# Performance work log

Hardware: AMD Instinct MI355X
Metric: run time of the kernel (lower is better)

The kernel has to match this reference:

```python
import jax, jax.numpy as jnp
import numpy as np

NUM_HEADS = 16


def _qdq(x):
    """Symmetric int8 fake-quant along the last axis (per-token for
    activations, per-output-channel for [out,in] weights). Equivalent math to
    int8 GEMM with dynamic scales: (x_q @ w_q.T) * sx * sw == qdq(x) @ qdq(w).T."""
    s = jnp.maximum(jnp.max(jnp.abs(x), axis=-1, keepdims=True) / 127.0, 1e-8)
    return jnp.clip(jnp.round(x / s), -127.0, 127.0) * s


def setup_inputs() -> dict:
    key = jax.random.key(0)
    ks = jax.random.split(key, 8)
    B, N, M, D = 2, 4096, 512, 2048
    w_std = 0.02
    return {
        "x": jax.random.normal(ks[0], (B, N, D), jnp.float32),
        "cond": jax.random.normal(ks[1], (B, M, D), jnp.float32),
        "wq": jax.random.normal(ks[2], (D, D), jnp.float32) * w_std,
        "bq": jax.random.normal(ks[3], (D,), jnp.float32) * w_std,
        "wkv": jax.random.normal(ks[4], (2 * D, D), jnp.float32) * w_std,
        "bkv": jax.random.normal(ks[5], (2 * D,), jnp.float32) * w_std,
        "wp": jax.random.normal(ks[6], (D, D), jnp.float32) * w_std,
        "bp": jax.random.normal(ks[7], (D,), jnp.float32) * w_std,
    }


def reference(x, cond, wq, bq, wkv, bkv, wp, bp):
    B, N, C = x.shape
    M = cond.shape[1]
    H = NUM_HEADS
    Dh = C // H

    # W8A8 dynamic-scale q projection (per-token act quant, per-channel weight quant)
    q = _qdq(x) @ _qdq(wq).T + bq                      # [B,N,C]
    # fp16-style kv projection
    kv = cond @ wkv.T + bkv                            # [B,M,2C]
    k, v = jnp.split(kv, 2, axis=-1)                   # view(...,2,H,Dh).unbind(2)

    q = q.reshape(B, N, H, Dh)
    k = k.reshape(B, M, H, Dh)
    v = v.reshape(B, M, H, Dh)

    scale = 1.0 / np.sqrt(Dh)
    attn = jax.nn.softmax(jnp.einsum('bnhd,bmhd->bhnm', q, k) * scale, axis=-1)
    o = jnp.einsum('bhnm,bmhd->bnhd', attn, v).reshape(B, N, C)

    # fused quant_sum (per-token requant of attention output) + W8A8 proj
    out = _qdq(o) @ _qdq(wp).T + bp                    # [B,N,C]
    return out
```

## Files before the change

### kernel.cpp

```cpp
#include <hip/hip_runtime.h>
#include <cstdint>
#include <cstddef>


typedef __bf16 bf16_t;
typedef __bf16 bf16x8 __attribute__((ext_vector_type(8)));
typedef float f32x4 __attribute__((ext_vector_type(4)));

__device__ __forceinline__ void gld16(void* lds, const void* g) {
    __builtin_amdgcn_global_load_lds(
        (__attribute__((address_space(1))) uint32_t*)(uintptr_t)g,
        (__attribute__((address_space(3))) uint32_t*)(uint32_t)(uintptr_t)lds,
        16, 0, 0);
}

__device__ __forceinline__ void load8(const float* p, int i, float* v) {
    const float4* p4 = (const float4*)p;
    float4 a = p4[2 * i], b = p4[2 * i + 1];
    v[0] = a.x; v[1] = a.y; v[2] = a.z; v[3] = a.w;
    v[4] = b.x; v[5] = b.y; v[6] = b.z; v[7] = b.w;
}
__device__ __forceinline__ void load8(const bf16_t* p, int i, float* v) {
    bf16x8 t = ((const bf16x8*)p)[i];
#pragma unroll
    for (int j = 0; j < 8; ++j) v[j] = (float)t[j];
}

template <int QUANT, typename T>
__global__ __launch_bounds__(256) void rowpack(const T* __restrict__ in,
                                               bf16_t* __restrict__ out, int K) {
    const int tid = threadIdx.x;
    const size_t row = blockIdx.x;
    const T* rp = in + row * (size_t)K;
    const int n8 = K >> 3;
    float scale = 1.0f;
    if (QUANT) {
        float m = 0.f;
        for (int i = tid; i < n8; i += 256) {
            float v[8];
            load8(rp, i, v);
#pragma unroll
            for (int j = 0; j < 8; ++j) m = fmaxf(m, fabsf(v[j]));
        }
        __shared__ float red[256];
        red[tid] = m;
        __syncthreads();
        for (int s = 128; s > 0; s >>= 1) {
            if (tid < s) red[tid] = fmaxf(red[tid], red[tid + s]);
            __syncthreads();
        }
        scale = fmaxf(red[0] * (1.0f / 127.0f), 1e-8f);
    }
    const int KT = K >> 5;
    const int p = (int)(row >> 7), c = ((int)row >> 4) & 7, lm = (int)row & 15;
    for (int i = tid; i < n8; i += 256) {
        const int col = i << 3;
        const int kt = col >> 5, quad = (col >> 3) & 3;
        float v[8];
        load8(rp, i, v);
        bf16x8 o8;
#pragma unroll
        for (int j = 0; j < 8; ++j) {
            float q = v[j];
            if (QUANT) {
                q = rintf(q / scale);
                q = fminf(127.f, fmaxf(-127.f, q)) * scale;
            }
            o8[j] = (bf16_t)q;
        }
        const size_t dst = ((size_t)(p * KT + kt) * 8 + c) * 512 + (quad * 16 + lm) * 8;
        *(bf16x8*)(out + dst) = o8;
    }
}

template <int MODE>
__device__ __forceinline__ void epi_store(void* C, int N, int row, int col, float v) {
    if (MODE == 1) {
        ((float*)C)[(size_t)row * N + col] = v;
    } else if (MODE == 0) {
        const int b = row >> 12, n = row & 4095;
        const int h = col >> 7, d = col & 127;
        const int p = n >> 6, mt = (n >> 4) & 3, lmq = n & 15;
        const int kq = d >> 5, qq = (d >> 3) & 3, jq = d & 7;
        const size_t idx = (((size_t)(b * 16 + h) * 64 + p) * 16 + kq * 4 + mt) * 512 +
                           (qq * 16 + lmq) * 8 + jq;
        ((bf16_t*)C)[idx] = (bf16_t)v;
    } else {
        const int b = row >> 9, m = row & 511;
        const int half = col >> 11, h = (col >> 7) & 15, d = col & 127;
        const int t8 = m >> 6;
        bf16_t* out = (bf16_t*)C;
        if (half == 0) {
            const int nt = (m >> 4) & 3, lmk = m & 15;
            const int kc = d >> 5, qk = (d >> 3) & 3, jk = d & 7;
            const size_t idx = (((size_t)(b * 16 + h) * 8 + t8) * 16 + kc * 4 + nt) * 512 +
                               (qk * 16 + lmk) * 8 + jk;
            out[idx] = (bf16_t)v;
        } else {
            const int kv2 = (m >> 5) & 1, qv = (m >> 3) & 3, jv = m & 7;
            const int ntv = d >> 4, lmv = d & 15;
            const size_t idx = 2097152 +
                (((size_t)(b * 16 + h) * 8 + t8) * 16 + kv2 * 8 + ntv) * 512 +
                (qv * 16 + lmv) * 8 + jv;
            out[idx] = (bf16_t)v;
        }
    }
}

__device__ __forceinline__ void stage_tile256(const bf16_t* __restrict__ A,
                                              const bf16_t* __restrict__ B,
                                              bf16_t* sa, bf16_t* sb,
                                              int pa, int pb, int KT, int t,
                                              int w, int l) {
#pragma unroll
    for (int it = 0; it < 4; ++it) {
        const int ci = w * 4 + it;
        const int h = ci >> 4, kt2 = (ci >> 3) & 1, c = ci & 7;
        const size_t ga = (((size_t)(pa + h) * KT + (2 * t + kt2)) * 8 + c) * 512 + l * 8;
        const size_t gb = (((size_t)(pb + h) * KT + (2 * t + kt2)) * 8 + c) * 512 + l * 8;
        gld16(sa + ci * 512, A + ga);
        gld16(sb + ci * 512, B + gb);
    }
}

template <int MODE>
__global__ __launch_bounds__(512, 1) void gemm_pk8(const bf16_t* __restrict__ A,
                                                   const bf16_t* __restrict__ B,
                                                   const float* __restrict__ bias,
                                                   void* __restrict__ C,
                                                   int N, int K) {
    __shared__ __align__(16) bf16_t sA[2][16384];
    __shared__ __align__(16) bf16_t sB[2][16384];

    const int tid = threadIdx.x;
    const int l = tid & 63, w = tid >> 6;
    const int lm = l & 15, quad = l >> 4;
    const int wm = w & 1, wn = w >> 1;

    const int nwg = gridDim.x;
    const int bid = blockIdx.x;
    const int s = (bid & 7) * (nwg >> 3) + (bid >> 3);
    const int bx = s & 7, by = s >> 3;

    const int KT = K >> 5;
    const int NT = K >> 6;
    const int pa = by * 2, pb = bx * 2;

    stage_tile256(A, B, sA[0], sB[0], pa, pb, KT, 0, w, l);
    __builtin_amdgcn_sched_barrier(0);
    stage_tile256(A, B, sA[1], sB[1], pa, pb, KT, 1, w, l);
    asm volatile("s_waitcnt vmcnt(8)" ::: "memory");
    __builtin_amdgcn_s_barrier();

    f32x4 acc[8][4] = {};

    for (int t = 0; t < NT; ++t) {
        const bf16_t* sa = sA[t & 1];
        const bf16_t* sb = sB[t & 1];
        bf16x8 bfr[4][2];
        bf16x8 af[2][2];

#pragma unroll
        for (int j = 0; j < 4; ++j)
#pragma unroll
            for (int k2 = 0; k2 < 2; ++k2)
                bfr[j][k2] = *(const bf16x8*)(
                    sb + ((((wn >> 1) * 2 + k2) * 8 + (wn & 1) * 4 + j) * 512) + l * 8);
#pragma unroll
        for (int ii = 0; ii < 2; ++ii)
#pragma unroll
            for (int k2 = 0; k2 < 2; ++k2)
                af[ii][k2] = *(const bf16x8*)(sa + (((wm * 2 + k2) * 8 + ii) * 512) + l * 8);
        __builtin_amdgcn_s_barrier();
        asm volatile("s_waitcnt lgkmcnt(0)" ::: "memory");
        __builtin_amdgcn_sched_barrier(0);
        __builtin_amdgcn_s_setprio(1);
#pragma unroll
        for (int ii = 0; ii < 2; ++ii)
#pragma unroll
            for (int j = 0; j < 4; ++j)
#pragma unroll
                for (int k2 = 0; k2 < 2; ++k2)
                    acc[ii][j] = __builtin_amdgcn_mfma_f32_16x16x32_bf16(
                        af[ii][k2], bfr[j][k2], acc[ii][j], 0, 0, 0);
        __builtin_amdgcn_s_setprio(0);
        __builtin_amdgcn_s_barrier();

#pragma unroll
        for (int q = 1; q <= 2; ++q) {
#pragma unroll
            for (int ii = 0; ii < 2; ++ii)
#pragma unroll
                for (int k2 = 0; k2 < 2; ++k2)
                    af[ii][k2] = *(const bf16x8*)(
                        sa + (((wm * 2 + k2) * 8 + (q * 2 + ii)) * 512) + l * 8);
            __builtin_amdgcn_s_barrier();
            asm volatile("s_waitcnt lgkmcnt(0)" ::: "memory");
            __builtin_amdgcn_sched_barrier(0);
            __builtin_amdgcn_s_setprio(1);
#pragma unroll
            for (int ii = 0; ii < 2; ++ii)
#pragma unroll
                for (int j = 0; j < 4; ++j)
#pragma unroll
                    for (int k2 = 0; k2 < 2; ++k2)
                        acc[q * 2 + ii][j] = __builtin_amdgcn_mfma_f32_16x16x32_bf16(
                            af[ii][k2], bfr[j][k2], acc[q * 2 + ii][j], 0, 0, 0);
            __builtin_amdgcn_s_setprio(0);
            __builtin_amdgcn_s_barrier();
        }

#pragma unroll
        for (int ii = 0; ii < 2; ++ii)
#pragma unroll
            for (int k2 = 0; k2 < 2; ++k2)
                af[ii][k2] = *(const bf16x8*)(
                    sa + (((wm * 2 + k2) * 8 + (6 + ii)) * 512) + l * 8);
        asm volatile("s_waitcnt lgkmcnt(0)" ::: "memory");
        __builtin_amdgcn_s_barrier();
        if (t + 2 < NT)
            stage_tile256(A, B, sA[t & 1], sB[t & 1], pa, pb, KT, t + 2, w, l);
        __builtin_amdgcn_sched_barrier(0);
        __builtin_amdgcn_s_setprio(1);
#pragma unroll
        for (int ii = 0; ii < 2; ++ii)
#pragma unroll
            for (int j = 0; j < 4; ++j)
#pragma unroll
                for (int k2 = 0; k2 < 2; ++k2)
                    acc[6 + ii][j] = __builtin_amdgcn_mfma_f32_16x16x32_bf16(
                        af[ii][k2], bfr[j][k2], acc[6 + ii][j], 0, 0, 0);
        __builtin_amdgcn_s_setprio(0);
        if (t + 2 < NT)
            asm volatile("s_waitcnt vmcnt(8)" ::: "memory");
        else
            asm volatile("s_waitcnt vmcnt(0)" ::: "memory");
        __builtin_amdgcn_s_barrier();
    }

#pragma unroll
    for (int i = 0; i < 8; ++i) {
#pragma unroll
        for (int j = 0; j < 4; ++j) {
            const int col = bx * 256 + wn * 64 + j * 16 + lm;
            const float bv = bias[col];
#pragma unroll
            for (int r = 0; r < 4; ++r) {
                const int row = by * 256 + wm * 128 + i * 16 + quad * 4 + r;
                epi_store<MODE>(C, N, row, col, acc[i][j][r] + bv);
            }
        }
    }
}

__global__ __launch_bounds__(256) void gemm_kv(const bf16_t* __restrict__ A,
                                               const bf16_t* __restrict__ B,
                                               const float* __restrict__ bias,
                                               bf16_t* __restrict__ C,
                                               int N, int K) {
    __shared__ __align__(16) bf16_t sA[4096];
    __shared__ __align__(16) bf16_t sB[8192];

    const int tid = threadIdx.x;
    const int l = tid & 63, w = tid >> 6;
    const int lm = l & 15, quad = l >> 4;
    const int wm = w & 1, wn = w >> 1;
    const int KT = K >> 5;
    const int p = blockIdx.y >> 1, hh = blockIdx.y & 1;
    const size_t aPan = (size_t)p * KT * 8 * 512;
    const size_t bBase = (size_t)blockIdx.x * KT * 8 * 512;

    f32x4 acc[2][4] = {};
    const int NIT = K >> 6;
    for (int kt = 0; kt < NIT; ++kt) {
        __syncthreads();
#pragma unroll
        for (int it = 0; it < 2; ++it) {
            const int lc = it * 4 + w;
            const int s = lc >> 2, cc = lc & 3;
            gld16(sA + lc * 512,
                  A + aPan + ((size_t)(kt * 2 + s) * 8 + hh * 4 + cc) * 512 + l * 8);
        }
#pragma unroll
        for (int it = 0; it < 4; ++it) {
            const int lc = it * 4 + w;
            gld16(sB + lc * 512, B + bBase + ((size_t)kt * 16 + lc) * 512 + l * 8);
        }
        __syncthreads();
#pragma unroll
        for (int s = 0; s < 2; ++s) {
            bf16x8 af[2], bfr[4];
#pragma unroll
            for (int i = 0; i < 2; ++i)
                af[i] = *(const bf16x8*)(sA + (s * 4 + wm * 2 + i) * 512 + l * 8);
#pragma unroll
            for (int j = 0; j < 4; ++j)
                bfr[j] = *(const bf16x8*)(sB + (s * 8 + wn * 4 + j) * 512 + l * 8);
#pragma unroll
            for (int i = 0; i < 2; ++i)
#pragma unroll
                for (int j = 0; j < 4; ++j)
                    acc[i][j] =
                        __builtin_amdgcn_mfma_f32_16x16x32_bf16(af[i], bfr[j], acc[i][j], 0, 0, 0);
        }
    }
#pragma unroll
    for (int i = 0; i < 2; ++i) {
#pragma unroll
        for (int j = 0; j < 4; ++j) {
            const int col = blockIdx.x * 128 + wn * 64 + j * 16 + lm;
            const float bv = bias[col];
#pragma unroll
            for (int r = 0; r < 4; ++r) {
                const int row = blockIdx.y * 64 + wm * 32 + i * 16 + quad * 4 + r;
                epi_store<2>(C, N, row, col, acc[i][j][r] + bv);
            }
        }
    }
}

__global__ __launch_bounds__(256, 2) void attn64(const bf16_t* __restrict__ qpk,
                                                 const bf16_t* __restrict__ kvpk,
                                                 bf16_t* __restrict__ o) {
    constexpr float SCALE = 0.08838834764831845f;
    __shared__ __align__(16) bf16_t sQP[8192];
    __shared__ __align__(16) bf16_t sKV[16384];
    __shared__ float redM[4][64];
    __shared__ float redS[4][64];

    const int tid = threadIdx.x;
    const int l = tid & 63, w = tid >> 6;
    const int lm = l & 15, quad = l >> 4;
    const int b = blockIdx.z, h = blockIdx.y;
    const int p = blockIdx.x;
    const int bh = b * 16 + h;
    const size_t qbase = ((size_t)bh * 64 + p) * 8192;
    const size_t kbase = (size_t)bh * 65536;
    const size_t vbase = 2097152 + (size_t)bh * 65536;

#pragma unroll
    for (int it = 0; it < 4; ++it) {
        const int c = it * 4 + w;
        gld16(sQP + c * 512, qpk + qbase + (size_t)c * 512 + l * 8);
    }
#pragma unroll
    for (int it = 0; it < 4; ++it) {
        const int c = it * 4 + w;
        gld16(sKV + c * 512, kvpk + kbase + (size_t)c * 512 + l * 8);
    }

    f32x4 sfr[8][4] = {};
#pragma unroll
    for (int sg = 0; sg < 8; ++sg) {
        if (sg < 7) {
            bf16_t* kn = sKV + (((sg + 1) & 1) << 13);
#pragma unroll
            for (int it = 0; it < 4; ++it) {
                const int c = it * 4 + w;
                gld16(kn + c * 512, kvpk + kbase + ((size_t)(sg + 1) * 16 + c) * 512 + l * 8);
            }
            asm volatile("s_waitcnt vmcnt(4)" ::: "memory");
        } else {
            asm volatile("s_waitcnt vmcnt(0)" ::: "memory");
        }
        __builtin_amdgcn_s_barrier();
        const bf16_t* kb = sKV + ((sg & 1) << 13);
        __builtin_amdgcn_s_setprio(1);
#pragma unroll
        for (int kc = 0; kc < 4; ++kc) {
            bf16x8 bb = *(const bf16x8*)(kb + (kc * 4 + w) * 512 + l * 8);
#pragma unroll
            for (int mt = 0; mt < 4; ++mt) {
                bf16x8 aa = *(const bf16x8*)(sQP + (kc * 4 + mt) * 512 + l * 8);
                sfr[sg][mt] =
                    __builtin_amdgcn_mfma_f32_16x16x32_bf16(aa, bb, sfr[sg][mt], 0, 0, 0);
            }
        }
        __builtin_amdgcn_s_setprio(0);
        asm volatile("s_waitcnt lgkmcnt(0)" ::: "memory");
        __builtin_amdgcn_s_barrier();
    }

#pragma unroll
    for (int it = 0; it < 4; ++it) {
        const int c = it * 4 + w;
        gld16(sKV + c * 512, kvpk + vbase + (size_t)c * 512 + l * 8);
    }

    float inv[4][4];
    {
        float mymax[4][4];
#pragma unroll
        for (int mt = 0; mt < 4; ++mt)
#pragma unroll
            for (int r = 0; r < 4; ++r) {
                float m = -3.0e38f;
#pragma unroll
                for (int t8 = 0; t8 < 8; ++t8) m = fmaxf(m, sfr[t8][mt][r]);
                m = fmaxf(m, __shfl_xor(m, 1));
                m = fmaxf(m, __shfl_xor(m, 2));
                m = fmaxf(m, __shfl_xor(m, 4));
                m = fmaxf(m, __shfl_xor(m, 8));
                mymax[mt][r] = m;
            }
        if (lm == 0) {
#pragma unroll
            for (int mt = 0; mt < 4; ++mt)
#pragma unroll
                for (int r = 0; r < 4; ++r)
                    redM[w][mt * 16 + quad * 4 + r] = mymax[mt][r];
        }
        asm volatile("s_waitcnt lgkmcnt(0)" ::: "memory");
        __builtin_amdgcn_s_barrier();
#pragma unroll
        for (int mt = 0; mt < 4; ++mt)
#pragma unroll
            for (int r = 0; r < 4; ++r) {
                const int row = mt * 16 + quad * 4 + r;
                const float M =
                    fmaxf(fmaxf(redM[0][row], redM[1][row]), fmaxf(redM[2][row], redM[3][row])) *
                    SCALE;
                float s = 0.f;
#pragma unroll
                for (int t8 = 0; t8 < 8; ++t8) {
                    const float pe = __expf(sfr[t8][mt][r] * SCALE - M);
                    sfr[t8][mt][r] = pe;
                    s += pe;
                }
                s += __shfl_xor(s, 1);
                s += __shfl_xor(s, 2);
                s += __shfl_xor(s, 4);
                s += __shfl_xor(s, 8);
                if (lm == 0) redS[w][row] = s;
            }
        asm volatile("s_waitcnt lgkmcnt(0)" ::: "memory");
        __builtin_amdgcn_s_barrier();
#pragma unroll
        for (int mt = 0; mt < 4; ++mt)
#pragma unroll
            for (int r = 0; r < 4; ++r) {
                const int row = mt * 16 + quad * 4 + r;
                inv[mt][r] = 1.f / (redS[0][row] + redS[1][row] + redS[2][row] + redS[3][row]);
            }
    }

    const int kvh = w >> 1;
    const int quadp = (w & 1) * 2 + (lm >> 3);
    const int jd = lm & 7;
#define PWRITE(sg_) do {                                                          \
    const int r8_ = ((sg_) & 1) * 8;                                              \
    _Pragma("unroll") for (int mt = 0; mt < 4; ++mt)                              \
    _Pragma("unroll") for (int r = 0; r < 4; ++r)                                 \
        sQP[(r8_ + mt * 2 + kvh) * 512 + (quadp * 16 + quad * 4 + r) * 8 + jd] =  \
            (bf16_t)sfr[sg_][mt][r];                                              \
} while (0)

    f32x4 oc[4][2] = {};
    PWRITE(0);
#pragma unroll
    for (int sg = 0; sg < 8; ++sg) {
        if (sg < 7) {
            bf16_t* vn = sKV + (((sg + 1) & 1) << 13);
#pragma unroll
            for (int it = 0; it < 4; ++it) {
                const int c = it * 4 + w;
                gld16(vn + c * 512, kvpk + vbase + ((size_t)(sg + 1) * 16 + c) * 512 + l * 8);
            }
            PWRITE(sg + 1);
            asm volatile("s_waitcnt vmcnt(4)" ::: "memory");
        } else {
            asm volatile("s_waitcnt vmcnt(0)" ::: "memory");
        }
        asm volatile("s_waitcnt lgkmcnt(0)" ::: "memory");
        __builtin_amdgcn_s_barrier();
        const bf16_t* vb = sKV + ((sg & 1) << 13);
        const bf16_t* pb = sQP + ((sg & 1) << 12);
        __builtin_amdgcn_s_setprio(1);
#pragma unroll
        for (int kvf2 = 0; kvf2 < 2; ++kvf2) {
            bf16x8 aa[4];
#pragma unroll
            for (int mt = 0; mt < 4; ++mt)
                aa[mt] = *(const bf16x8*)(pb + (mt * 2 + kvf2) * 512 + l * 8);
#pragma unroll
            for (int ni = 0; ni < 2; ++ni) {
                bf16x8 bb = *(const bf16x8*)(vb + (kvf2 * 8 + w * 2 + ni) * 512 + l * 8);
#pragma unroll
                for (int mt = 0; mt < 4; ++mt)
                    oc[mt][ni] =
                        __builtin_amdgcn_mfma_f32_16x16x32_bf16(aa[mt], bb, oc[mt][ni], 0, 0, 0);
            }
        }
        __builtin_amdgcn_s_setprio(0);
        asm volatile("s_waitcnt lgkmcnt(0)" ::: "memory");
        __builtin_amdgcn_s_barrier();
    }
#undef PWRITE

#pragma unroll
    for (int mt = 0; mt < 4; ++mt)
#pragma unroll
        for (int ni = 0; ni < 2; ++ni)
#pragma unroll
            for (int r = 0; r < 4; ++r) {
                const int row = mt * 16 + quad * 4 + r;
                const int d = w * 32 + ni * 16 + lm;
                o[((size_t)b * 4096 + p * 64 + row) * 2048 + h * 128 + d] =
                    (bf16_t)(oc[mt][ni][r] * inv[mt][r]);
            }
}

extern "C" void kernel_launch(void* const* d_in, const int* in_sizes, int n_in,
                              void* d_out, int out_size, void* d_ws, size_t ws_size,
                              hipStream_t stream) {
    (void)in_sizes; (void)n_in; (void)out_size; (void)ws_size;
    const float* x    = (const float*)d_in[0];
    const float* cond = (const float*)d_in[1];
    const float* wq   = (const float*)d_in[2];
    const float* bq   = (const float*)d_in[3];
    const float* wkv  = (const float*)d_in[4];
    const float* bkv  = (const float*)d_in[5];
    const float* wp   = (const float*)d_in[6];
    const float* bp   = (const float*)d_in[7];

    const size_t MB = 1ull << 20;
    uint8_t* ws = (uint8_t*)d_ws;
    bf16_t* qxpk   = (bf16_t*)(ws + 0);
    bf16_t* qpk    = (bf16_t*)(ws + 32 * MB);
    bf16_t* wqpk   = (bf16_t*)(ws + 64 * MB);
    bf16_t* wkvpk  = (bf16_t*)(ws + 72 * MB);
    bf16_t* wppk   = (bf16_t*)(ws + 88 * MB);
    bf16_t* condpk = (bf16_t*)(ws + 96 * MB);
    bf16_t* kvpk   = (bf16_t*)(ws + 100 * MB);
    bf16_t* o_nat  = qxpk;
    bf16_t* opk    = qpk;

    dim3 blk(256);
    rowpack<1, float><<<8192, blk, 0, stream>>>(x, qxpk, 2048);
    rowpack<1, float><<<2048, blk, 0, stream>>>(wq, wqpk, 2048);
    rowpack<1, float><<<2048, blk, 0, stream>>>(wp, wppk, 2048);
    rowpack<0, float><<<1024, blk, 0, stream>>>(cond, condpk, 2048);
    rowpack<0, float><<<4096, blk, 0, stream>>>(wkv, wkvpk, 2048);
    gemm_pk8<0><<<dim3(256), dim3(512), 0, stream>>>(qxpk, wqpk, bq, qpk, 2048, 2048);
    gemm_kv<<<dim3(32, 16), blk, 0, stream>>>(condpk, wkvpk, bkv, kvpk, 4096, 2048);
    attn64<<<dim3(64, 16, 2), blk, 0, stream>>>(qpk, kvpk, o_nat);
    rowpack<1, bf16_t><<<8192, blk, 0, stream>>>(o_nat, opk, 2048);
    gemm_pk8<1><<<dim3(256), dim3(512), 0, stream>>>(opk, wppk, bp, (float*)d_out, 2048, 2048);
}
```

Before: 513.0 us.

## Triple-buffer K/V stream in attention kernel and hoist Q fragments to registers

Replaces the two-stage K/V shared-memory double buffer with a three-stage ring that keeps two tiles in flight, and runs K and V as one continuous prefetch stream so V loads start during the QK phase. Q fragments are loaded once into registers instead of being re-read from shared memory on every K tile. The cost is more shared memory (48KB for sKV) and extra VGPRs for the Q fragments, which may lower occupancy under the 2-block launch bound.

```diff
diff --git a/kernel.cpp b/kernel.cpp
--- a/kernel.cpp
+++ b/kernel.cpp
@@ -324,7 +324,7 @@
                                                  bf16_t* __restrict__ o) {
     constexpr float SCALE = 0.08838834764831845f;
     __shared__ __align__(16) bf16_t sQP[8192];
-    __shared__ __align__(16) bf16_t sKV[16384];
+    __shared__ __align__(16) bf16_t sKV[24576];
     __shared__ float redM[4][64];
     __shared__ float redS[4][64];
 
@@ -338,53 +338,55 @@
     const size_t kbase = (size_t)bh * 65536;
     const size_t vbase = 2097152 + (size_t)bh * 65536;
 
+    auto issue = [&](int n) {
+        bf16_t* dst = sKV + (n % 3) * 8192;
+        const size_t src = (n < 8) ? kbase + (size_t)n * 8192
+                                   : vbase + (size_t)(n - 8) * 8192;
+#pragma unroll
+        for (int it = 0; it < 4; ++it) {
+            const int c = it * 4 + w;
+            gld16(dst + c * 512, kvpk + src + (size_t)c * 512 + l * 8);
+        }
+    };
+
 #pragma unroll
     for (int it = 0; it < 4; ++it) {
         const int c = it * 4 + w;
         gld16(sQP + c * 512, qpk + qbase + (size_t)c * 512 + l * 8);
     }
-#pragma unroll
-    for (int it = 0; it < 4; ++it) {
-        const int c = it * 4 + w;
-        gld16(sKV + c * 512, kvpk + kbase + (size_t)c * 512 + l * 8);
-    }
-
+    issue(0);
+    __builtin_amdgcn_sched_barrier(0);
+    issue(1);
+
+    bf16x8 qf[4][4];
     f32x4 sfr[8][4] = {};
+
 #pragma unroll
     for (int sg = 0; sg < 8; ++sg) {
-        if (sg < 7) {
-            bf16_t* kn = sKV + (((sg + 1) & 1) << 13);
-#pragma unroll
-            for (int it = 0; it < 4; ++it) {
-                const int c = it * 4 + w;
-                gld16(kn + c * 512, kvpk + kbase + ((size_t)(sg + 1) * 16 + c) * 512 + l * 8);
-            }
-            asm volatile("s_waitcnt vmcnt(4)" ::: "memory");
-        } else {
-            asm volatile("s_waitcnt vmcnt(0)" ::: "memory");
-        }
-        __builtin_amdgcn_s_barrier();
-        const bf16_t* kb = sKV + ((sg & 1) << 13);
+        issue(sg + 2);
+        asm volatile("s_waitcnt vmcnt(8)" ::: "memory");
+        __builtin_amdgcn_s_barrier();
+        __builtin_amdgcn_sched_barrier(0);
+        const bf16_t* kb = sKV + (sg % 3) * 8192;
+        if (sg == 0) {
+#pragma unroll
+            for (int kc = 0; kc < 4; ++kc)
+#pragma unroll
+                for (int mt = 0; mt < 4; ++mt)
+                    qf[kc][mt] = *(const bf16x8*)(sQP + (kc * 4 + mt) * 512 + l * 8);
+        }
         __builtin_amdgcn_s_setprio(1);
 #pragma unroll
         for (int kc = 0; kc < 4; ++kc) {
             bf16x8 bb = *(const bf16x8*)(kb + (kc * 4 + w) * 512 + l * 8);
 #pragma unroll
-            for (int mt = 0; mt < 4; ++mt) {
-                bf16x8 aa = *(const bf16x8*)(sQP + (kc * 4 + mt) * 512 + l * 8);
+            for (int mt = 0; mt < 4; ++mt)
                 sfr[sg][mt] =
-                    __builtin_amdgcn_mfma_f32_16x16x32_bf16(aa, bb, sfr[sg][mt], 0, 0, 0);
-            }
+                    __builtin_amdgcn_mfma_f32_16x16x32_bf16(qf[kc][mt], bb, sfr[sg][mt], 0, 0, 0);
         }
         __builtin_amdgcn_s_setprio(0);
         asm volatile("s_waitcnt lgkmcnt(0)" ::: "memory");
         __builtin_amdgcn_s_barrier();
-    }
-
-#pragma unroll
-    for (int it = 0; it < 4; ++it) {
-        const int c = it * 4 + w;
-        gld16(sKV + c * 512, kvpk + vbase + (size_t)c * 512 + l * 8);
     }
 
     float inv[4][4];
@@ -459,21 +461,18 @@
     PWRITE(0);
 #pragma unroll
     for (int sg = 0; sg < 8; ++sg) {
-        if (sg < 7) {
-            bf16_t* vn = sKV + (((sg + 1) & 1) << 13);
-#pragma unroll
-            for (int it = 0; it < 4; ++it) {
-                const int c = it * 4 + w;
-                gld16(vn + c * 512, kvpk + vbase + ((size_t)(sg + 1) * 16 + c) * 512 + l * 8);
-            }
-            PWRITE(sg + 1);
+        if (sg < 6) issue(sg + 10);
+        if (sg < 7) PWRITE(sg + 1);
+        if (sg < 6)
+            asm volatile("s_waitcnt vmcnt(8)" ::: "memory");
+        else if (sg == 6)
             asm volatile("s_waitcnt vmcnt(4)" ::: "memory");
-        } else {
+        else
             asm volatile("s_waitcnt vmcnt(0)" ::: "memory");
-        }
-        asm volatile("s_waitcnt lgkmcnt(0)" ::: "memory");
-        __builtin_amdgcn_s_barrier();
-        const bf16_t* vb = sKV + ((sg & 1) << 13);
+        asm volatile("s_waitcnt lgkmcnt(0)" ::: "memory");
+        __builtin_amdgcn_s_barrier();
+        __builtin_amdgcn_sched_barrier(0);
+        const bf16_t* vb = sKV + ((sg + 8) % 3) * 8192;
         const bf16_t* pb = sQP + ((sg & 1) << 12);
         __builtin_amdgcn_s_setprio(1);
 #pragma unroll
```

Result: no change. 512.6 us (-0.1%).

## Deepen K/V prefetch in attention, drop per-step barriers, raise occupancy

Applied to the files above, without the earlier changes.

The attention kernel now prefetches K and V tiles two stages ahead. It relies on each wave loading the same LDS chunks it later reads, so most block-wide barriers in the QK and PV loops can be removed. Operand fragments are read into registers before the next tile is issued. Softmax probabilities are packed into bf16 pairs in 32-bit registers instead of staying in the fp32 score array, and launch bounds ask for 3 blocks per CU instead of 2. The goal is to hide global-load latency and cut synchronisation stalls, at the cost of higher register pressure and a possible spill under the tighter occupancy target.

```diff
diff --git a/kernel.cpp b/kernel.cpp
--- a/kernel.cpp
+++ b/kernel.cpp
@@ -24,6 +24,14 @@
     bf16x8 t = ((const bf16x8*)p)[i];
 #pragma unroll
     for (int j = 0; j < 8; ++j) v[j] = (float)t[j];
+}
+
+__device__ __forceinline__ uint32_t bf16bits(float f) {
+    bf16_t h = (bf16_t)f;
+    return (uint32_t)__builtin_bit_cast(unsigned short, h);
+}
+__device__ __forceinline__ bf16_t bits2bf16(uint32_t u) {
+    return __builtin_bit_cast(bf16_t, (unsigned short)(u & 0xffffu));
 }
 
 template <int QUANT, typename T>
@@ -319,7 +327,7 @@
     }
 }
 
-__global__ __launch_bounds__(256, 2) void attn64(const bf16_t* __restrict__ qpk,
+__global__ __launch_bounds__(256, 3) void attn64(const bf16_t* __restrict__ qpk,
                                                  const bf16_t* __restrict__ kvpk,
                                                  bf16_t* __restrict__ o) {
     constexpr float SCALE = 0.08838834764831845f;
@@ -338,56 +346,71 @@
     const size_t kbase = (size_t)bh * 65536;
     const size_t vbase = 2097152 + (size_t)bh * 65536;
 
+    auto issueK = [&](int n) {
+        bf16_t* dst = sKV + ((n & 1) << 13);
+#pragma unroll
+        for (int it = 0; it < 4; ++it) {
+            const int c = it * 4 + w;
+            gld16(dst + c * 512, kvpk + kbase + ((size_t)n * 16 + c) * 512 + l * 8);
+        }
+    };
+    auto issueV = [&](int n) {
+        bf16_t* dst = sKV + ((n & 1) << 13);
+#pragma unroll
+        for (int it = 0; it < 4; ++it) {
+            const int c = ((it >> 1) << 3) + w * 2 + (it & 1);
+            gld16(dst + c * 512, kvpk + vbase + ((size_t)n * 16 + c) * 512 + l * 8);
+        }
+    };
+
 #pragma unroll
     for (int it = 0; it < 4; ++it) {
         const int c = it * 4 + w;
         gld16(sQP + c * 512, qpk + qbase + (size_t)c * 512 + l * 8);
     }
-#pragma unroll
-    for (int it = 0; it < 4; ++it) {
-        const int c = it * 4 + w;
-        gld16(sKV + c * 512, kvpk + kbase + (size_t)c * 512 + l * 8);
-    }
+    __builtin_amdgcn_sched_barrier(0);
+    issueK(0);
+    __builtin_amdgcn_sched_barrier(0);
+    issueK(1);
+    asm volatile("s_waitcnt vmcnt(8)" ::: "memory");
+    __builtin_amdgcn_s_barrier();
 
     f32x4 sfr[8][4] = {};
 #pragma unroll
     for (int sg = 0; sg < 8; ++sg) {
-        if (sg < 7) {
-            bf16_t* kn = sKV + (((sg + 1) & 1) << 13);
-#pragma unroll
-            for (int it = 0; it < 4; ++it) {
-                const int c = it * 4 + w;
-                gld16(kn + c * 512, kvpk + kbase + ((size_t)(sg + 1) * 16 + c) * 512 + l * 8);
-            }
+        if (sg < 7)
             asm volatile("s_waitcnt vmcnt(4)" ::: "memory");
-        } else {
+        else
             asm volatile("s_waitcnt vmcnt(0)" ::: "memory");
-        }
-        __builtin_amdgcn_s_barrier();
         const bf16_t* kb = sKV + ((sg & 1) << 13);
+        bf16x8 bb[4];
+#pragma unroll
+        for (int kc = 0; kc < 4; ++kc)
+            bb[kc] = *(const bf16x8*)(kb + (kc * 4 + w) * 512 + l * 8);
+        asm volatile("s_waitcnt lgkmcnt(0)" ::: "memory");
+        if (sg < 6) issueK(sg + 2);
+        __builtin_amdgcn_sched_barrier(0);
         __builtin_amdgcn_s_setprio(1);
 #pragma unroll
         for (int kc = 0; kc < 4; ++kc) {
-            bf16x8 bb = *(const bf16x8*)(kb + (kc * 4 + w) * 512 + l * 8);
 #pragma unroll
             for (int mt = 0; mt < 4; ++mt) {
                 bf16x8 aa = *(const bf16x8*)(sQP + (kc * 4 + mt) * 512 + l * 8);
                 sfr[sg][mt] =
-                    __builtin_amdgcn_mfma_f32_16x16x32_bf16(aa, bb, sfr[sg][mt], 0, 0, 0);
+                    __builtin_amdgcn_mfma_f32_16x16x32_bf16(aa, bb[kc], sfr[sg][mt], 0, 0, 0);
             }
         }
         __builtin_amdgcn_s_setprio(0);
-        asm volatile("s_waitcnt lgkmcnt(0)" ::: "memory");
-        __builtin_amdgcn_s_barrier();
-    }
-
-#pragma unroll
-    for (int it = 0; it < 4; ++it) {
-        const int c = it * 4 + w;
-        gld16(sKV + c * 512, kvpk + vbase + (size_t)c * 512 + l * 8);
-    }
+    }
+
+    asm volatile("s_waitcnt lgkmcnt(0)" ::: "memory");
+    __builtin_amdgcn_s_barrier();
+    issueV(0);
+    __builtin_amdgcn_sched_barrier(0);
+    issueV(1);
 
     float inv[4][4];
+    uint32_t pw[8][8];
     {
         float mymax[4][4];
 #pragma unroll
@@ -424,7 +447,11 @@
 #pragma unroll
                 for (int t8 = 0; t8 < 8; ++t8) {
                     const float pe = __expf(sfr[t8][mt][r] * SCALE - M);
-                    sfr[t8][mt][r] = pe;
+                    const int idx = mt * 4 + r;
+                    if (idx & 1)
+                        pw[t8][idx >> 1] |= bf16bits(pe) << 16;
+                    else
+                        pw[t8][idx >> 1] = bf16bits(pe);
                     s += pe;
                 }
                 s += __shfl_xor(s, 1);
@@ -450,50 +477,51 @@
 #define PWRITE(sg_) do {                                                          \
     const int r8_ = ((sg_) & 1) * 8;                                              \
     _Pragma("unroll") for (int mt = 0; mt < 4; ++mt)                              \
-    _Pragma("unroll") for (int r = 0; r < 4; ++r)                                 \
+    _Pragma("unroll") for (int r = 0; r < 4; ++r) {                               \
+        const int idx_ = mt * 4 + r;                                              \
+        const uint32_t u_ = pw[sg_][idx_ >> 1];                                   \
         sQP[(r8_ + mt * 2 + kvh) * 512 + (quadp * 16 + quad * 4 + r) * 8 + jd] =  \
-            (bf16_t)sfr[sg_][mt][r];                                              \
+            bits2bf16((idx_ & 1) ? (u_ >> 16) : u_);                              \
+    }                                                                             \
 } while (0)
 
     f32x4 oc[4][2] = {};
     PWRITE(0);
+    asm volatile("s_waitcnt lgkmcnt(0)" ::: "memory");
+    __builtin_amdgcn_s_barrier();
 #pragma unroll
     for (int sg = 0; sg < 8; ++sg) {
-        if (sg < 7) {
-            bf16_t* vn = sKV + (((sg + 1) & 1) << 13);
-#pragma unroll
-            for (int it = 0; it < 4; ++it) {
-                const int c = it * 4 + w;
-                gld16(vn + c * 512, kvpk + vbase + ((size_t)(sg + 1) * 16 + c) * 512 + l * 8);
-            }
-            PWRITE(sg + 1);
+        if (sg < 7) PWRITE(sg + 1);
+        if (sg < 7)
             asm volatile("s_waitcnt vmcnt(4)" ::: "memory");
-        } else {
+        else
             asm volatile("s_waitcnt vmcnt(0)" ::: "memory");
-        }
-        asm volatile("s_waitcnt lgkmcnt(0)" ::: "memory");
-        __builtin_amdgcn_s_barrier();
         const bf16_t* vb = sKV + ((sg & 1) << 13);
         const bf16_t* pb = sQP + ((sg & 1) << 12);
+        bf16x8 aa2[2][4], bb2[2][2];
+#pragma unroll
+        for (int kvf2 = 0; kvf2 < 2; ++kvf2) {
+#pragma unroll
+            for (int mt = 0; mt < 4; ++mt)
+                aa2[kvf2][mt] = *(const bf16x8*)(pb + (mt * 2 + kvf2) * 512 + l * 8);
+#pragma unroll
+            for (int ni = 0; ni < 2; ++ni)
+                bb2[kvf2][ni] = *(const bf16x8*)(vb + (kvf2 * 8 + w * 2 + ni) * 512 + l * 8);
+        }
+        asm volatile("s_waitcnt lgkmcnt(0)" ::: "memory");
+        if (sg < 7) __builtin_amdgcn_s_barrier();
+        if (sg < 6) issueV(sg + 2);
+        __builtin_amdgcn_sched_barrier(0);
         __builtin_amdgcn_s_setprio(1);
 #pragma unroll
-        for (int kvf2 = 0; kvf2 < 2; ++kvf2) {
-            bf16x8 aa[4];
-#pragma unroll
-            for (int mt = 0; mt < 4; ++mt)
-                aa[mt] = *(const bf16x8*)(pb + (mt * 2 + kvf2) * 512 + l * 8);
-#pragma unroll
-            for (int ni = 0; ni < 2; ++ni) {
-                bf16x8 bb = *(const bf16x8*)(vb + (kvf2 * 8 + w * 2 + ni) * 512 + l * 8);
+        for (int kvf2 = 0; kvf2 < 2; ++kvf2)
+#pragma unroll
+            for (int ni = 0; ni < 2; ++ni)
 #pragma unroll
                 for (int mt = 0; mt < 4; ++mt)
-                    oc[mt][ni] =
-                        __builtin_amdgcn_mfma_f32_16x16x32_bf16(aa[mt], bb, oc[mt][ni], 0, 0, 0);
-            }
-        }
+                    oc[mt][ni] = __builtin_amdgcn_mfma_f32_16x16x32_bf16(
+                        aa2[kvf2][mt], bb2[kvf2][ni], oc[mt][ni], 0, 0, 0);
         __builtin_amdgcn_s_setprio(0);
-        asm volatile("s_waitcnt lgkmcnt(0)" ::: "memory");
-        __builtin_amdgcn_s_barrier();
     }
 #undef PWRITE
 
```

Result: slower. 585.4 us (+14.1%).
